# Kernel optimization log

Measured on AMD Instinct MI355X. Metric: run time of the kernel, lower is better.

Reference implementation:

```python
import jax, jax.numpy as jnp
import numpy as np

EMBED_DIM = 1024
NUM_HEADS = 16
HEAD_DIM = EMBED_DIM // NUM_HEADS
B, T = 2, 2048


def setup_inputs() -> dict:
    key = jax.random.key(0)
    ks = jax.random.split(key, 9)
    s = 1.0 / np.sqrt(EMBED_DIM)
    return {
        "x": jax.random.normal(ks[0], (B, T, EMBED_DIM), dtype=jnp.float32),
        "W_q": jax.random.uniform(ks[1], (EMBED_DIM, EMBED_DIM), jnp.float32, -s, s),
        "b_q": jax.random.uniform(ks[2], (EMBED_DIM,), jnp.float32, -s, s),
        "W_k": jax.random.uniform(ks[3], (EMBED_DIM, EMBED_DIM), jnp.float32, -s, s),
        "b_k": jax.random.uniform(ks[4], (EMBED_DIM,), jnp.float32, -s, s),
        "W_v": jax.random.uniform(ks[5], (EMBED_DIM, EMBED_DIM), jnp.float32, -s, s),
        "b_v": jax.random.uniform(ks[6], (EMBED_DIM,), jnp.float32, -s, s),
        "W_o": jax.random.uniform(ks[7], (EMBED_DIM, EMBED_DIM), jnp.float32, -s, s),
        "b_o": jax.random.uniform(ks[8], (EMBED_DIM,), jnp.float32, -s, s),
    }


def reference(x, W_q, b_q, W_k, b_k, W_v, b_v, W_o, b_o):
    Bv, Tv, C = x.shape
    # QKV projections (torch Linear: x @ W.T + b); split into heads -> (B,H,T,Dh)
    def proj(W, b):
        return (x @ W.T + b).reshape(Bv, Tv, NUM_HEADS, HEAD_DIM).transpose(0, 2, 1, 3)
    q, k, v = proj(W_q, b_q), proj(W_k, b_k), proj(W_v, b_v)
    scale = 1.0 / np.sqrt(HEAD_DIM).astype(np.float32)
    scores = jnp.einsum("bhqd,bhkd->bhqk", q, k) * scale  # (B,H,T,T)
    causal = jnp.tril(jnp.ones((Tv, Tv), dtype=bool))
    scores = jnp.where(causal, scores, -jnp.inf)
    attn = jax.nn.softmax(scores, axis=-1)
    # dropout is identity in eval / p=0
    out = jnp.einsum("bhqk,bhkd->bhqd", attn, v)  # (B,H,T,Dh)
    out = out.transpose(0, 2, 1, 3).reshape(Bv, Tv, C)
    return out @ W_o.T + b_o
```

## Files before the change

### kernel.cpp

```cpp
#include <hip/hip_runtime.h>
#include <hip/hip_bf16.h>


typedef __bf16 bf16;
typedef __attribute__((ext_vector_type(8))) __bf16 bf16x8;
typedef __attribute__((ext_vector_type(4))) __bf16 bf16x4;
typedef __attribute__((ext_vector_type(4))) float floatx4;
typedef __attribute__((ext_vector_type(8))) unsigned short us8;
typedef __attribute__((ext_vector_type(4))) unsigned short us4;

#define LOG2E 1.44269504088896340736f

__device__ __forceinline__ void gl2lds16(const void* g, void* l) {
  __builtin_amdgcn_global_load_lds((const __attribute__((address_space(1))) void*)g,
                                   (__attribute__((address_space(3))) void*)l, 16, 0, 0);
}

__global__ __launch_bounds__(256) void cast_all(
    const float* __restrict__ x, const float* __restrict__ wq,
    const float* __restrict__ wk, const float* __restrict__ wv,
    const float* __restrict__ wo, bf16* __restrict__ dst)
{
  const size_t M1 = (size_t)1 << 20;
  size_t i4 = ((size_t)blockIdx.x * 256 + threadIdx.x) * 4;
  const float* src = x;
  size_t off = i4;
  if (i4 >= 4 * M1) {
    size_t r = i4 - 4 * M1;
    int seg = (int)(r >> 20);
    off = r & (M1 - 1);
    src = (seg == 0) ? wq : (seg == 1) ? wk : (seg == 2) ? wv : wo;
  }
  float4 f = *(const float4*)(src + off);
  bf16x4 o = { (bf16)f.x, (bf16)f.y, (bf16)f.z, (bf16)f.w };
  *(bf16x4*)(dst + i4) = o;
}

template<bool F32OUT, bool QKV, int BN>
__global__ __launch_bounds__(256, 2) void gemm_bt(
    const bf16* __restrict__ A, const bf16* __restrict__ Wb,
    const float* __restrict__ bq, const float* __restrict__ bk,
    const float* __restrict__ bv, void* __restrict__ outb,
    int M, int N, int K, float qscale)
{
  __shared__ bf16 As[128 * 32];
  __shared__ bf16 Bs[BN * 32];
  const int tid = threadIdx.x;
  const int lane = tid & 63;
  const int wid = tid >> 6;
  const int l15 = lane & 15, l4 = lane >> 4;
  constexpr int I = (BN == 128) ? 4 : 2;
  const int wr = (BN == 128) ? (wid >> 1) : wid;
  const int wc = (BN == 128) ? (wid & 1) : 0;

  const bf16* W;
  const float* bias;
  float osc = 1.0f;
  int n0;
  bf16* outh;
  float* outf;
  if (QKV) {
    int mat = blockIdx.x >> 3;
    n0 = (blockIdx.x & 7) << 7;
    W = Wb + ((size_t)mat << 20);
    bias = (mat == 0) ? bq : (mat == 1 ? bk : bv);
    if (mat == 0) osc = qscale;
    outh = (bf16*)outb + ((size_t)mat << 22);
    outf = nullptr;
  } else {
    n0 = blockIdx.x * BN;
    W = Wb;
    bias = bq;
    outf = (float*)outb;
    outh = nullptr;
  }
  const int m0 = blockIdx.y << 7;

  floatx4 acc[I][4] = {};

  for (int k0 = 0; k0 < K; k0 += 32) {
#pragma unroll
    for (int it = 0; it < 2; ++it) {
      int c = it * 256 + tid;
      int row = c >> 2, kof = (c & 3) << 3;
      gl2lds16(A + (size_t)(m0 + row) * K + k0 + kof, As + c * 8);
    }
#pragma unroll
    for (int it = 0; it < BN / 64; ++it) {
      int c = it * 256 + tid;
      int row = c >> 2, kof = (c & 3) << 3;
      gl2lds16(W + (size_t)(n0 + row) * K + k0 + kof, Bs + c * 8);
    }
    __syncthreads();
    bf16x8 af[I], bfr[4];
#pragma unroll
    for (int i = 0; i < I; ++i)
      af[i] = *(const bf16x8*)(As + (wr * (I * 16) + i * 16 + l15) * 32 + l4 * 8);
#pragma unroll
    for (int j = 0; j < 4; ++j)
      bfr[j] = *(const bf16x8*)(Bs + (wc * 64 + j * 16 + l15) * 32 + l4 * 8);
#pragma unroll
    for (int i = 0; i < I; ++i)
#pragma unroll
      for (int j = 0; j < 4; ++j)
        acc[i][j] = __builtin_amdgcn_mfma_f32_16x16x32_bf16(af[i], bfr[j], acc[i][j], 0, 0, 0);
    __syncthreads();
  }

#pragma unroll
  for (int j = 0; j < 4; ++j) {
    int col = n0 + wc * 64 + j * 16 + l15;
    float bv_ = bias[col];
#pragma unroll
    for (int i = 0; i < I; ++i) {
#pragma unroll
      for (int rg = 0; rg < 4; ++rg) {
        int row = m0 + wr * (I * 16) + i * 16 + l4 * 4 + rg;
        float v = (acc[i][j][rg] + bv_) * osc;
        if (F32OUT) outf[(size_t)row * N + col] = v;
        else        outh[(size_t)row * N + col] = (bf16)v;
      }
    }
  }
}

__global__ __launch_bounds__(256) void transpose_v(
    const bf16* __restrict__ V, bf16* __restrict__ Vt)
{
  __shared__ bf16 tile[64 * 68];
  const int tid = threadIdx.x;
  const int t0 = blockIdx.x << 6;
  const int bh = blockIdx.y;
  const bf16* vp = V + ((size_t)(bh >> 4) * 2048) * 1024 + (bh & 15) * 64;
  bf16* op = Vt + ((size_t)bh << 17);

#pragma unroll
  for (int it = 0; it < 2; ++it) {
    int c = it * 256 + tid;
    int row = c >> 3, gcol = (c & 7) * 8;
    bf16x8 v8 = *(const bf16x8*)(vp + (size_t)(t0 + row) * 1024 + gcol);
    *(us4*)(&tile[row * 68 + gcol])     = *(us4*)&v8;
    *(us4*)(&tile[row * 68 + gcol + 4]) = ((us4*)&v8)[1];
  }
  __syncthreads();
#pragma unroll
  for (int it = 0; it < 2; ++it) {
    int u = it * 256 + tid;
    int d = u >> 3, ch = u & 7;
    us8 r;
#pragma unroll
    for (int jj = 0; jj < 8; ++jj)
      r[jj] = *(const unsigned short*)&tile[(ch * 8 + jj) * 68 + d];
    *(us8*)(op + (size_t)d * 2048 + t0 + ch * 8) = r;
  }
}

__global__ __launch_bounds__(256, 3) void attn_kernel(
    const bf16* __restrict__ Q, const bf16* __restrict__ Kg,
    const bf16* __restrict__ Vt, bf16* __restrict__ AO)
{
  constexpr int T = 2048, C = 1024;
  __shared__ bf16 Ks[2][64 * 64];
  __shared__ bf16 Vts[2][64 * 64];
  __shared__ bf16 Ps[4][16 * 72];

  const int tid = threadIdx.x;
  const int lane = tid & 63;
  const int w = tid >> 6;
  const int l15 = lane & 15, l4 = lane >> 4;

  const int p = blockIdx.x;
  const int bh = blockIdx.y;
  const size_t base = ((size_t)(bh >> 4) * T) * C + (bh & 15) * 64;
  const bf16* vtb = Vt + ((size_t)bh << 17);

  const bf16 one_h = (bf16)1.0f;
  const bf16x8 ones = {one_h, one_h, one_h, one_h, one_h, one_h, one_h, one_h};

  auto stageK = [&](int j0, int bufi) {
#pragma unroll
    for (int it = 0; it < 2; ++it) {
      int c = it * 256 + tid;
      int row = c >> 3, s = (c & 7) ^ (row & 7);
      gl2lds16(Kg + base + (size_t)(j0 + row) * C + s * 8, &Ks[bufi][c * 8]);
    }
  };
  auto stageV = [&](int j0, int bufi) {
#pragma unroll
    for (int it = 0; it < 2; ++it) {
      int c = it * 256 + tid;
      int row = c >> 3, s = (c & 7) ^ (row & 7);
      gl2lds16(vtb + ((size_t)row << 11) + j0 + s * 8, &Vts[bufi][c * 8]);
    }
  };

  const int qts[2] = { p, 31 - p };
  int g = 0;
  stageK(0, 0);
  stageV(0, 0);

  for (int seg = 0; seg < 2; ++seg) {
    const int qt = qts[seg];
    const int q0 = qt << 6;
    const int nkt = qt + 1;

    bf16x8 aq[2];
    {
      const bf16* qp = Q + base + (size_t)(q0 + w * 16 + l15) * C + l4 * 8;
      aq[0] = *(const bf16x8*)(qp);
      aq[1] = *(const bf16x8*)(qp + 32);
    }
    floatx4 o[4] = {};
    floatx4 lacc = {0.f, 0.f, 0.f, 0.f};
    float mrow[4] = {-1e38f, -1e38f, -1e38f, -1e38f};

    for (int jt = 0; jt < nkt; ++jt, ++g) {
      __syncthreads();
      const int cur = g & 1;
      if (jt + 1 < nkt) {
        stageK((jt + 1) << 6, cur ^ 1);
        stageV((jt + 1) << 6, cur ^ 1);
      } else if (seg == 0) {
        stageK(0, cur ^ 1);
        stageV(0, cur ^ 1);
      }

      floatx4 s4[4] = {};
#pragma unroll
      for (int kk = 0; kk < 2; ++kk) {
        bf16x8 bk8[4];
#pragma unroll
        for (int tj = 0; tj < 4; ++tj) {
          int r = tj * 16 + l15;
          int sl = (kk * 4 + l4) ^ (r & 7);
          bk8[tj] = *(const bf16x8*)(&Ks[cur][r * 64 + sl * 8]);
        }
#pragma unroll
        for (int tj = 0; tj < 4; ++tj)
          s4[tj] = __builtin_amdgcn_mfma_f32_16x16x32_bf16(aq[kk], bk8[tj], s4[tj], 0, 0, 0);
      }

      if (jt == nkt - 1) {
        const int j0 = jt << 6;
        int qrowb = q0 + w * 16 + l4 * 4;
#pragma unroll
        for (int tj = 0; tj < 4; ++tj) {
          int kcol = j0 + tj * 16 + l15;
#pragma unroll
          for (int rg = 0; rg < 4; ++rg)
            if (kcol > qrowb + rg) s4[tj][rg] = -3e38f;
        }
      }

#pragma unroll
      for (int rg = 0; rg < 4; ++rg) {
        float mx = fmaxf(fmaxf(s4[0][rg], s4[1][rg]), fmaxf(s4[2][rg], s4[3][rg]));
#pragma unroll
        for (int off = 1; off < 16; off <<= 1)
          mx = fmaxf(mx, __shfl_xor(mx, off, 64));
        float mnew = fmaxf(mrow[rg], mx);
        float al = __builtin_amdgcn_exp2f(mrow[rg] - mnew);
        mrow[rg] = mnew;
#pragma unroll
        for (int tj = 0; tj < 4; ++tj)
          s4[tj][rg] = __builtin_amdgcn_exp2f(s4[tj][rg] - mnew);
        lacc[rg] *= al;
#pragma unroll
        for (int td = 0; td < 4; ++td)
          o[td][rg] *= al;
      }

#pragma unroll
      for (int tj = 0; tj < 4; ++tj)
#pragma unroll
        for (int rg = 0; rg < 4; ++rg)
          Ps[w][(l4 * 4 + rg) * 72 + tj * 16 + l15] = (bf16)s4[tj][rg];

#pragma unroll
      for (int tk = 0; tk < 2; ++tk) {
        bf16x8 ap = *(const bf16x8*)(&Ps[w][l15 * 72 + tk * 32 + l4 * 8]);
        lacc = __builtin_amdgcn_mfma_f32_16x16x32_bf16(ap, ones, lacc, 0, 0, 0);
#pragma unroll
        for (int td = 0; td < 4; ++td) {
          int r = td * 16 + l15;
          int sl = (tk * 4 + l4) ^ (r & 7);
          bf16x8 bv8 = *(const bf16x8*)(&Vts[cur][r * 64 + sl * 8]);
          o[td] = __builtin_amdgcn_mfma_f32_16x16x32_bf16(ap, bv8, o[td], 0, 0, 0);
        }
      }
    }

#pragma unroll
    for (int rg = 0; rg < 4; ++rg) {
      float inv = 1.0f / lacc[rg];
      int qrow = q0 + w * 16 + l4 * 4 + rg;
#pragma unroll
      for (int td = 0; td < 4; ++td)
        AO[base + (size_t)qrow * C + td * 16 + l15] = (bf16)(o[td][rg] * inv);
    }
  }
}

extern "C" void kernel_launch(void* const* d_in, const int* in_sizes, int n_in,
                              void* d_out, int out_size, void* d_ws, size_t ws_size,
                              hipStream_t stream) {
  const float* x  = (const float*)d_in[0];
  const float* Wq = (const float*)d_in[1];
  const float* bq = (const float*)d_in[2];
  const float* Wk = (const float*)d_in[3];
  const float* bk = (const float*)d_in[4];
  const float* Wv = (const float*)d_in[5];
  const float* bv = (const float*)d_in[6];
  const float* Wo = (const float*)d_in[7];
  const float* bo = (const float*)d_in[8];

  bf16* ws = (bf16*)d_ws;
  const size_t M1 = (size_t)1 << 20;
  bf16* xb  = ws;
  bf16* Vtp = ws;
  bf16* wqb = ws + 4 * M1;
  bf16* wob = ws + 7 * M1;
  bf16* Qp  = ws + 8 * M1;
  bf16* AOp = ws + 20 * M1;

  cast_all<<<8192, 256, 0, stream>>>(x, Wq, Wk, Wv, Wo, ws);
  gemm_bt<false, true, 128><<<dim3(24, 32), 256, 0, stream>>>(
      xb, wqb, bq, bk, bv, (void*)Qp, 4096, 1024, 1024, 0.125f * LOG2E);
  transpose_v<<<dim3(32, 32), 256, 0, stream>>>(Qp + 8 * M1, Vtp);
  attn_kernel<<<dim3(16, 32), 256, 0, stream>>>(Qp, Qp + 4 * M1, Vtp, AOp);
  gemm_bt<true, false, 64><<<dim3(16, 32), 256, 0, stream>>>(
      AOp, wob, bo, nullptr, nullptr, d_out, 4096, 1024, 1024, 1.0f);
}
```

Before: 206.9 us.

## Use 128-row query tiles per block with transposed S MFMA and register row sums

The attention kernel now gives each block one 128-row query tile, so each wave handles 32 query rows, instead of pairing two 64-row tiles per block. Each staged K/V tile is reused by twice as many query rows. Blocks are ordered longest-first to balance the causal workload. S is computed as K·Q^T so each lane holds a query column, which lets row max and sum use two shuffles and accumulate the sum in registers instead of using a ones-MFMA. The cost is more registers (launch bounds lowered from 3 to 2 blocks per CU) and waves that sit idle on fully masked tiles.

```diff
diff --git a/kernel.cpp b/kernel.cpp
--- a/kernel.cpp
+++ b/kernel.cpp
@@ -155,27 +155,39 @@
   }
 }
 
-__global__ __launch_bounds__(256, 3) void attn_kernel(
+__global__ __launch_bounds__(256, 2) void attn_kernel(
     const bf16* __restrict__ Q, const bf16* __restrict__ Kg,
     const bf16* __restrict__ Vt, bf16* __restrict__ AO)
 {
   constexpr int T = 2048, C = 1024;
   __shared__ bf16 Ks[2][64 * 64];
   __shared__ bf16 Vts[2][64 * 64];
-  __shared__ bf16 Ps[4][16 * 72];
+  __shared__ bf16 Ps[4][32 * 72];
 
   const int tid = threadIdx.x;
   const int lane = tid & 63;
   const int w = tid >> 6;
   const int l15 = lane & 15, l4 = lane >> 4;
 
-  const int p = blockIdx.x;
-  const int bh = blockIdx.y;
+  const int u = blockIdx.x;
+  const int bh = u & 31;
+  const int p = u >> 5;
+  const int qt = (p < 8) ? (15 - p) : (p - 8);
+  const int q0 = qt << 7;
   const size_t base = ((size_t)(bh >> 4) * T) * C + (bh & 15) * 64;
   const bf16* vtb = Vt + ((size_t)bh << 17);
 
-  const bf16 one_h = (bf16)1.0f;
-  const bf16x8 ones = {one_h, one_h, one_h, one_h, one_h, one_h, one_h, one_h};
+  bf16x8 qf[2][2];
+#pragma unroll
+  for (int tq = 0; tq < 2; ++tq) {
+    const bf16* qp = Q + base + (size_t)(q0 + w * 32 + tq * 16 + l15) * C + l4 * 8;
+    qf[tq][0] = *(const bf16x8*)(qp);
+    qf[tq][1] = *(const bf16x8*)(qp + 32);
+  }
+
+  floatx4 o[2][4] = {};
+  float mrow[2] = {-1e38f, -1e38f};
+  float lrow[2] = {0.f, 0.f};
 
   auto stageK = [&](int j0, int bufi) {
 #pragma unroll
@@ -194,111 +206,128 @@
     }
   };
 
-  const int qts[2] = { p, 31 - p };
-  int g = 0;
+  const int nkt = 2 * qt + 2;
   stageK(0, 0);
   stageV(0, 0);
 
-  for (int seg = 0; seg < 2; ++seg) {
-    const int qt = qts[seg];
-    const int q0 = qt << 6;
-    const int nkt = qt + 1;
-
-    bf16x8 aq[2];
-    {
-      const bf16* qp = Q + base + (size_t)(q0 + w * 16 + l15) * C + l4 * 8;
-      aq[0] = *(const bf16x8*)(qp);
-      aq[1] = *(const bf16x8*)(qp + 32);
-    }
-    floatx4 o[4] = {};
-    floatx4 lacc = {0.f, 0.f, 0.f, 0.f};
-    float mrow[4] = {-1e38f, -1e38f, -1e38f, -1e38f};
-
-    for (int jt = 0; jt < nkt; ++jt, ++g) {
-      __syncthreads();
-      const int cur = g & 1;
-      if (jt + 1 < nkt) {
-        stageK((jt + 1) << 6, cur ^ 1);
-        stageV((jt + 1) << 6, cur ^ 1);
-      } else if (seg == 0) {
-        stageK(0, cur ^ 1);
-        stageV(0, cur ^ 1);
-      }
-
-      floatx4 s4[4] = {};
+  for (int jt = 0; jt < nkt; ++jt) {
+    __syncthreads();
+    const int cur = jt & 1;
+    if (jt + 1 < nkt) {
+      stageK((jt + 1) << 6, cur ^ 1);
+      stageV((jt + 1) << 6, cur ^ 1);
+    }
+    const int j0 = jt << 6;
+    const int qwave = q0 + w * 32;
+    if (j0 <= qwave + 31) {
+      floatx4 s4[4][2] = {};
 #pragma unroll
       for (int kk = 0; kk < 2; ++kk) {
-        bf16x8 bk8[4];
+        bf16x8 kf[4];
 #pragma unroll
         for (int tj = 0; tj < 4; ++tj) {
           int r = tj * 16 + l15;
           int sl = (kk * 4 + l4) ^ (r & 7);
-          bk8[tj] = *(const bf16x8*)(&Ks[cur][r * 64 + sl * 8]);
+          kf[tj] = *(const bf16x8*)(&Ks[cur][r * 64 + sl * 8]);
         }
 #pragma unroll
         for (int tj = 0; tj < 4; ++tj)
-          s4[tj] = __builtin_amdgcn_mfma_f32_16x16x32_bf16(aq[kk], bk8[tj], s4[tj], 0, 0, 0);
-      }
-
-      if (jt == nkt - 1) {
-        const int j0 = jt << 6;
-        int qrowb = q0 + w * 16 + l4 * 4;
+#pragma unroll
+          for (int tq = 0; tq < 2; ++tq)
+            s4[tj][tq] = __builtin_amdgcn_mfma_f32_16x16x32_bf16(kf[tj], qf[tq][kk], s4[tj][tq], 0, 0, 0);
+      }
+
+      if (j0 + 63 > qwave) {
 #pragma unroll
         for (int tj = 0; tj < 4; ++tj) {
-          int kcol = j0 + tj * 16 + l15;
+          int j = j0 + tj * 16 + l4 * 4;
+#pragma unroll
+          for (int tq = 0; tq < 2; ++tq) {
+            int q = qwave + tq * 16 + l15;
+#pragma unroll
+            for (int rg = 0; rg < 4; ++rg)
+              if (j + rg > q) s4[tj][tq][rg] = -3e38f;
+          }
+        }
+      }
+
+      float al[2];
+#pragma unroll
+      for (int tq = 0; tq < 2; ++tq) {
+        float mx = -3e38f;
+#pragma unroll
+        for (int tj = 0; tj < 4; ++tj)
 #pragma unroll
           for (int rg = 0; rg < 4; ++rg)
-            if (kcol > qrowb + rg) s4[tj][rg] = -3e38f;
-        }
-      }
-
-#pragma unroll
-      for (int rg = 0; rg < 4; ++rg) {
-        float mx = fmaxf(fmaxf(s4[0][rg], s4[1][rg]), fmaxf(s4[2][rg], s4[3][rg]));
-#pragma unroll
-        for (int off = 1; off < 16; off <<= 1)
-          mx = fmaxf(mx, __shfl_xor(mx, off, 64));
-        float mnew = fmaxf(mrow[rg], mx);
-        float al = __builtin_amdgcn_exp2f(mrow[rg] - mnew);
-        mrow[rg] = mnew;
+            mx = fmaxf(mx, s4[tj][tq][rg]);
+        mx = fmaxf(mx, __shfl_xor(mx, 16, 64));
+        mx = fmaxf(mx, __shfl_xor(mx, 32, 64));
+        float mnew = fmaxf(mrow[tq], mx);
+        al[tq] = __builtin_amdgcn_exp2f(mrow[tq] - mnew);
+        mrow[tq] = mnew;
+        float psum = 0.f;
 #pragma unroll
         for (int tj = 0; tj < 4; ++tj)
-          s4[tj][rg] = __builtin_amdgcn_exp2f(s4[tj][rg] - mnew);
-        lacc[rg] *= al;
-#pragma unroll
-        for (int td = 0; td < 4; ++td)
-          o[td][rg] *= al;
-      }
-
-#pragma unroll
-      for (int tj = 0; tj < 4; ++tj)
-#pragma unroll
-        for (int rg = 0; rg < 4; ++rg)
-          Ps[w][(l4 * 4 + rg) * 72 + tj * 16 + l15] = (bf16)s4[tj][rg];
+#pragma unroll
+          for (int rg = 0; rg < 4; ++rg) {
+            float e = __builtin_amdgcn_exp2f(s4[tj][tq][rg] - mnew);
+            s4[tj][tq][rg] = e;
+            psum += e;
+          }
+        psum += __shfl_xor(psum, 16, 64);
+        psum += __shfl_xor(psum, 32, 64);
+        lrow[tq] = lrow[tq] * al[tq] + psum;
+      }
+
+#pragma unroll
+      for (int tq = 0; tq < 2; ++tq)
+#pragma unroll
+        for (int tj = 0; tj < 4; ++tj) {
+          bf16x4 pk = { (bf16)s4[tj][tq][0], (bf16)s4[tj][tq][1],
+                        (bf16)s4[tj][tq][2], (bf16)s4[tj][tq][3] };
+          *(bf16x4*)(&Ps[w][(tq * 16 + l15) * 72 + tj * 16 + l4 * 4]) = pk;
+        }
+
+#pragma unroll
+      for (int tm = 0; tm < 2; ++tm)
+#pragma unroll
+        for (int rg = 0; rg < 4; ++rg) {
+          float aO = __shfl(al[tm], l4 * 4 + rg, 64);
+#pragma unroll
+          for (int td = 0; td < 4; ++td)
+            o[tm][td][rg] *= aO;
+        }
 
 #pragma unroll
       for (int tk = 0; tk < 2; ++tk) {
-        bf16x8 ap = *(const bf16x8*)(&Ps[w][l15 * 72 + tk * 32 + l4 * 8]);
-        lacc = __builtin_amdgcn_mfma_f32_16x16x32_bf16(ap, ones, lacc, 0, 0, 0);
+        bf16x8 pf[2];
+#pragma unroll
+        for (int tm = 0; tm < 2; ++tm)
+          pf[tm] = *(const bf16x8*)(&Ps[w][(tm * 16 + l15) * 72 + tk * 32 + l4 * 8]);
 #pragma unroll
         for (int td = 0; td < 4; ++td) {
           int r = td * 16 + l15;
           int sl = (tk * 4 + l4) ^ (r & 7);
-          bf16x8 bv8 = *(const bf16x8*)(&Vts[cur][r * 64 + sl * 8]);
-          o[td] = __builtin_amdgcn_mfma_f32_16x16x32_bf16(ap, bv8, o[td], 0, 0, 0);
-        }
-      }
-    }
-
+          bf16x8 vf = *(const bf16x8*)(&Vts[cur][r * 64 + sl * 8]);
+#pragma unroll
+          for (int tm = 0; tm < 2; ++tm)
+            o[tm][td] = __builtin_amdgcn_mfma_f32_16x16x32_bf16(pf[tm], vf, o[tm][td], 0, 0, 0);
+        }
+      }
+    }
+  }
+
+  float inv[2] = { 1.0f / lrow[0], 1.0f / lrow[1] };
+#pragma unroll
+  for (int tm = 0; tm < 2; ++tm)
 #pragma unroll
     for (int rg = 0; rg < 4; ++rg) {
-      float inv = 1.0f / lacc[rg];
-      int qrow = q0 + w * 16 + l4 * 4 + rg;
+      float iv = __shfl(inv[tm], l4 * 4 + rg, 64);
+      int qrow = q0 + w * 32 + tm * 16 + l4 * 4 + rg;
 #pragma unroll
       for (int td = 0; td < 4; ++td)
-        AO[base + (size_t)qrow * C + td * 16 + l15] = (bf16)(o[td][rg] * inv);
-    }
-  }
+        AO[base + (size_t)qrow * C + td * 16 + l15] = (bf16)(o[tm][td][rg] * iv);
+    }
 }
 
 extern "C" void kernel_launch(void* const* d_in, const int* in_sizes, int n_in,
@@ -327,7 +356,7 @@
   gemm_bt<false, true, 128><<<dim3(24, 32), 256, 0, stream>>>(
       xb, wqb, bq, bk, bv, (void*)Qp, 4096, 1024, 1024, 0.125f * LOG2E);
   transpose_v<<<dim3(32, 32), 256, 0, stream>>>(Qp + 8 * M1, Vtp);
-  attn_kernel<<<dim3(16, 32), 256, 0, stream>>>(Qp, Qp + 4 * M1, Vtp, AOp);
+  attn_kernel<<<512, 256, 0, stream>>>(Qp, Qp + 4 * M1, Vtp, AOp);
   gemm_bt<true, false, 64><<<dim3(16, 32), 256, 0, stream>>>(
       AOp, wob, bo, nullptr, nullptr, d_out, 4096, 1024, 1024, 1.0f);
 }
```

Result: no change. 204.4 us (-1.2%).

## Fuse V transpose into QKV GEMM epilogue and restructure attention grid

Applied to the files above, without the earlier changes.

The QKV projection GEMM now writes the V output directly in transposed per-head layout, which removes the separate transpose kernel launch and its extra read and write of V. The attention kernel swaps its paired-q-tile work assignment for one q-tile per block over 1024 blocks, longest tiles first. It also computes S^T and O^T with swapped MFMA operands so row statistics reduce with two shuffles, and it replaces the ones-MFMA row sum with register sums. The risks are strided 8-byte scattered stores for Vt in the GEMM epilogue and load imbalance without tile pairing.

```diff
diff --git a/kernel.cpp b/kernel.cpp
--- a/kernel.cpp
+++ b/kernel.cpp
@@ -6,8 +6,6 @@
 typedef __attribute__((ext_vector_type(8))) __bf16 bf16x8;
 typedef __attribute__((ext_vector_type(4))) __bf16 bf16x4;
 typedef __attribute__((ext_vector_type(4))) float floatx4;
-typedef __attribute__((ext_vector_type(8))) unsigned short us8;
-typedef __attribute__((ext_vector_type(4))) unsigned short us4;
 
 #define LOG2E 1.44269504088896340736f
 
@@ -41,7 +39,7 @@
     const bf16* __restrict__ A, const bf16* __restrict__ Wb,
     const float* __restrict__ bq, const float* __restrict__ bk,
     const float* __restrict__ bv, void* __restrict__ outb,
-    int M, int N, int K, float qscale)
+    bf16* __restrict__ vt, int M, int N, int K, float qscale)
 {
   __shared__ bf16 As[128 * 32];
   __shared__ bf16 Bs[BN * 32];
@@ -56,11 +54,11 @@
   const bf16* W;
   const float* bias;
   float osc = 1.0f;
-  int n0;
+  int n0, mat = 0;
   bf16* outh;
   float* outf;
   if (QKV) {
-    int mat = blockIdx.x >> 3;
+    mat = blockIdx.x >> 3;
     n0 = (blockIdx.x & 7) << 7;
     W = Wb + ((size_t)mat << 20);
     bias = (mat == 0) ? bq : (mat == 1 ? bk : bv);
@@ -107,6 +105,25 @@
     __syncthreads();
   }
 
+  if (QKV && mat == 2) {
+#pragma unroll
+    for (int j = 0; j < 4; ++j) {
+      int col = n0 + wc * 64 + j * 16 + l15;
+      float bv_ = bias[col];
+      int h = col >> 6, d = col & 63;
+#pragma unroll
+      for (int i = 0; i < I; ++i) {
+        int row = m0 + wr * (I * 16) + i * 16 + l4 * 4;
+        int bb = row >> 11, t = row & 2047;
+        bf16x4 pk;
+#pragma unroll
+        for (int rg = 0; rg < 4; ++rg) pk[rg] = (bf16)(acc[i][j][rg] + bv_);
+        *(bf16x4*)(vt + (((size_t)(bb * 16 + h)) << 17) + ((size_t)d << 11) + t) = pk;
+      }
+    }
+    return;
+  }
+
 #pragma unroll
   for (int j = 0; j < 4; ++j) {
     int col = n0 + wc * 64 + j * 16 + l15;
@@ -121,37 +138,6 @@
         else        outh[(size_t)row * N + col] = (bf16)v;
       }
     }
-  }
-}
-
-__global__ __launch_bounds__(256) void transpose_v(
-    const bf16* __restrict__ V, bf16* __restrict__ Vt)
-{
-  __shared__ bf16 tile[64 * 68];
-  const int tid = threadIdx.x;
-  const int t0 = blockIdx.x << 6;
-  const int bh = blockIdx.y;
-  const bf16* vp = V + ((size_t)(bh >> 4) * 2048) * 1024 + (bh & 15) * 64;
-  bf16* op = Vt + ((size_t)bh << 17);
-
-#pragma unroll
-  for (int it = 0; it < 2; ++it) {
-    int c = it * 256 + tid;
-    int row = c >> 3, gcol = (c & 7) * 8;
-    bf16x8 v8 = *(const bf16x8*)(vp + (size_t)(t0 + row) * 1024 + gcol);
-    *(us4*)(&tile[row * 68 + gcol])     = *(us4*)&v8;
-    *(us4*)(&tile[row * 68 + gcol + 4]) = ((us4*)&v8)[1];
-  }
-  __syncthreads();
-#pragma unroll
-  for (int it = 0; it < 2; ++it) {
-    int u = it * 256 + tid;
-    int d = u >> 3, ch = u & 7;
-    us8 r;
-#pragma unroll
-    for (int jj = 0; jj < 8; ++jj)
-      r[jj] = *(const unsigned short*)&tile[(ch * 8 + jj) * 68 + d];
-    *(us8*)(op + (size_t)d * 2048 + t0 + ch * 8) = r;
   }
 }
 
@@ -162,20 +148,31 @@
   constexpr int T = 2048, C = 1024;
   __shared__ bf16 Ks[2][64 * 64];
   __shared__ bf16 Vts[2][64 * 64];
-  __shared__ bf16 Ps[4][16 * 72];
+  __shared__ bf16 Ps[4][16 * 80];
 
   const int tid = threadIdx.x;
   const int lane = tid & 63;
   const int w = tid >> 6;
   const int l15 = lane & 15, l4 = lane >> 4;
 
-  const int p = blockIdx.x;
-  const int bh = blockIdx.y;
+  const int u = blockIdx.x;
+  const int bh = u & 31;
+  const int qt = 31 - (u >> 5);
+  const int q0 = qt << 6;
   const size_t base = ((size_t)(bh >> 4) * T) * C + (bh & 15) * 64;
   const bf16* vtb = Vt + ((size_t)bh << 17);
 
-  const bf16 one_h = (bf16)1.0f;
-  const bf16x8 ones = {one_h, one_h, one_h, one_h, one_h, one_h, one_h, one_h};
+  const int q = q0 + w * 16 + l15;
+
+  bf16x8 qf[2];
+  {
+    const bf16* qp = Q + base + (size_t)q * C + l4 * 8;
+    qf[0] = *(const bf16x8*)(qp);
+    qf[1] = *(const bf16x8*)(qp + 32);
+  }
+
+  floatx4 o[4] = {};
+  float mrow = -1e38f, lrow = 0.f;
 
   auto stageK = [&](int j0, int bufi) {
 #pragma unroll
@@ -194,110 +191,100 @@
     }
   };
 
-  const int qts[2] = { p, 31 - p };
-  int g = 0;
+  const int nkt = qt + 1;
   stageK(0, 0);
   stageV(0, 0);
 
-  for (int seg = 0; seg < 2; ++seg) {
-    const int qt = qts[seg];
-    const int q0 = qt << 6;
-    const int nkt = qt + 1;
-
-    bf16x8 aq[2];
-    {
-      const bf16* qp = Q + base + (size_t)(q0 + w * 16 + l15) * C + l4 * 8;
-      aq[0] = *(const bf16x8*)(qp);
-      aq[1] = *(const bf16x8*)(qp + 32);
-    }
-    floatx4 o[4] = {};
-    floatx4 lacc = {0.f, 0.f, 0.f, 0.f};
-    float mrow[4] = {-1e38f, -1e38f, -1e38f, -1e38f};
-
-    for (int jt = 0; jt < nkt; ++jt, ++g) {
-      __syncthreads();
-      const int cur = g & 1;
-      if (jt + 1 < nkt) {
-        stageK((jt + 1) << 6, cur ^ 1);
-        stageV((jt + 1) << 6, cur ^ 1);
-      } else if (seg == 0) {
-        stageK(0, cur ^ 1);
-        stageV(0, cur ^ 1);
-      }
-
-      floatx4 s4[4] = {};
-#pragma unroll
-      for (int kk = 0; kk < 2; ++kk) {
-        bf16x8 bk8[4];
-#pragma unroll
-        for (int tj = 0; tj < 4; ++tj) {
-          int r = tj * 16 + l15;
-          int sl = (kk * 4 + l4) ^ (r & 7);
-          bk8[tj] = *(const bf16x8*)(&Ks[cur][r * 64 + sl * 8]);
-        }
-#pragma unroll
-        for (int tj = 0; tj < 4; ++tj)
-          s4[tj] = __builtin_amdgcn_mfma_f32_16x16x32_bf16(aq[kk], bk8[tj], s4[tj], 0, 0, 0);
-      }
-
-      if (jt == nkt - 1) {
-        const int j0 = jt << 6;
-        int qrowb = q0 + w * 16 + l4 * 4;
-#pragma unroll
-        for (int tj = 0; tj < 4; ++tj) {
-          int kcol = j0 + tj * 16 + l15;
-#pragma unroll
-          for (int rg = 0; rg < 4; ++rg)
-            if (kcol > qrowb + rg) s4[tj][rg] = -3e38f;
-        }
-      }
-
+  for (int jt = 0; jt < nkt; ++jt) {
+    __syncthreads();
+    const int cur = jt & 1;
+    if (jt + 1 < nkt) {
+      stageK((jt + 1) << 6, cur ^ 1);
+      stageV((jt + 1) << 6, cur ^ 1);
+    }
+    const int j0 = jt << 6;
+
+    floatx4 s4[4] = {};
+#pragma unroll
+    for (int kk = 0; kk < 2; ++kk) {
+      bf16x8 kf[4];
+#pragma unroll
+      for (int tj = 0; tj < 4; ++tj) {
+        int r = tj * 16 + l15;
+        int sl = (kk * 4 + l4) ^ (r & 7);
+        kf[tj] = *(const bf16x8*)(&Ks[cur][r * 64 + sl * 8]);
+      }
+#pragma unroll
+      for (int tj = 0; tj < 4; ++tj)
+        s4[tj] = __builtin_amdgcn_mfma_f32_16x16x32_bf16(kf[tj], qf[kk], s4[tj], 0, 0, 0);
+    }
+
+    if (jt == nkt - 1) {
+#pragma unroll
+      for (int tj = 0; tj < 4; ++tj) {
+        int j = j0 + tj * 16 + l4 * 4;
+#pragma unroll
+        for (int rg = 0; rg < 4; ++rg)
+          if (j + rg > q) s4[tj][rg] = -3e38f;
+      }
+    }
+
+    float mx = -3e38f;
+#pragma unroll
+    for (int tj = 0; tj < 4; ++tj)
+#pragma unroll
+      for (int rg = 0; rg < 4; ++rg)
+        mx = fmaxf(mx, s4[tj][rg]);
+    mx = fmaxf(mx, __shfl_xor(mx, 16, 64));
+    mx = fmaxf(mx, __shfl_xor(mx, 32, 64));
+    float mnew = fmaxf(mrow, mx);
+    float al = __builtin_amdgcn_exp2f(mrow - mnew);
+    mrow = mnew;
+    float psum = 0.f;
+#pragma unroll
+    for (int tj = 0; tj < 4; ++tj)
 #pragma unroll
       for (int rg = 0; rg < 4; ++rg) {
-        float mx = fmaxf(fmaxf(s4[0][rg], s4[1][rg]), fmaxf(s4[2][rg], s4[3][rg]));
-#pragma unroll
-        for (int off = 1; off < 16; off <<= 1)
-          mx = fmaxf(mx, __shfl_xor(mx, off, 64));
-        float mnew = fmaxf(mrow[rg], mx);
-        float al = __builtin_amdgcn_exp2f(mrow[rg] - mnew);
-        mrow[rg] = mnew;
-#pragma unroll
-        for (int tj = 0; tj < 4; ++tj)
-          s4[tj][rg] = __builtin_amdgcn_exp2f(s4[tj][rg] - mnew);
-        lacc[rg] *= al;
-#pragma unroll
-        for (int td = 0; td < 4; ++td)
-          o[td][rg] *= al;
-      }
-
-#pragma unroll
-      for (int tj = 0; tj < 4; ++tj)
-#pragma unroll
-        for (int rg = 0; rg < 4; ++rg)
-          Ps[w][(l4 * 4 + rg) * 72 + tj * 16 + l15] = (bf16)s4[tj][rg];
-
-#pragma unroll
-      for (int tk = 0; tk < 2; ++tk) {
-        bf16x8 ap = *(const bf16x8*)(&Ps[w][l15 * 72 + tk * 32 + l4 * 8]);
-        lacc = __builtin_amdgcn_mfma_f32_16x16x32_bf16(ap, ones, lacc, 0, 0, 0);
-#pragma unroll
-        for (int td = 0; td < 4; ++td) {
-          int r = td * 16 + l15;
-          int sl = (tk * 4 + l4) ^ (r & 7);
-          bf16x8 bv8 = *(const bf16x8*)(&Vts[cur][r * 64 + sl * 8]);
-          o[td] = __builtin_amdgcn_mfma_f32_16x16x32_bf16(ap, bv8, o[td], 0, 0, 0);
-        }
-      }
-    }
-
-#pragma unroll
-    for (int rg = 0; rg < 4; ++rg) {
-      float inv = 1.0f / lacc[rg];
-      int qrow = q0 + w * 16 + l4 * 4 + rg;
-#pragma unroll
-      for (int td = 0; td < 4; ++td)
-        AO[base + (size_t)qrow * C + td * 16 + l15] = (bf16)(o[td][rg] * inv);
-    }
+        float e = __builtin_amdgcn_exp2f(s4[tj][rg] - mnew);
+        s4[tj][rg] = e;
+        psum += e;
+      }
+    psum += __shfl_xor(psum, 16, 64);
+    psum += __shfl_xor(psum, 32, 64);
+    lrow = lrow * al + psum;
+
+#pragma unroll
+    for (int tj = 0; tj < 4; ++tj) {
+      bf16x4 pk = { (bf16)s4[tj][0], (bf16)s4[tj][1],
+                    (bf16)s4[tj][2], (bf16)s4[tj][3] };
+      *(bf16x4*)(&Ps[w][l15 * 80 + tj * 16 + l4 * 4]) = pk;
+    }
+
+#pragma unroll
+    for (int td = 0; td < 4; ++td)
+#pragma unroll
+      for (int rg = 0; rg < 4; ++rg)
+        o[td][rg] *= al;
+
+#pragma unroll
+    for (int tk = 0; tk < 2; ++tk) {
+      bf16x8 pf = *(const bf16x8*)(&Ps[w][l15 * 80 + tk * 32 + l4 * 8]);
+#pragma unroll
+      for (int td = 0; td < 4; ++td) {
+        int r = td * 16 + l15;
+        int sl = (tk * 4 + l4) ^ (r & 7);
+        bf16x8 vf = *(const bf16x8*)(&Vts[cur][r * 64 + sl * 8]);
+        o[td] = __builtin_amdgcn_mfma_f32_16x16x32_bf16(vf, pf, o[td], 0, 0, 0);
+      }
+    }
+  }
+
+  float inv = 1.0f / lrow;
+#pragma unroll
+  for (int td = 0; td < 4; ++td) {
+    bf16x4 ok = { (bf16)(o[td][0] * inv), (bf16)(o[td][1] * inv),
+                  (bf16)(o[td][2] * inv), (bf16)(o[td][3] * inv) };
+    *(bf16x4*)(AO + base + (size_t)q * C + td * 16 + l4 * 4) = ok;
   }
 }
 
@@ -317,17 +304,16 @@
   bf16* ws = (bf16*)d_ws;
   const size_t M1 = (size_t)1 << 20;
   bf16* xb  = ws;
-  bf16* Vtp = ws;
   bf16* wqb = ws + 4 * M1;
   bf16* wob = ws + 7 * M1;
   bf16* Qp  = ws + 8 * M1;
+  bf16* Vtp = ws + 16 * M1;
   bf16* AOp = ws + 20 * M1;
 
   cast_all<<<8192, 256, 0, stream>>>(x, Wq, Wk, Wv, Wo, ws);
   gemm_bt<false, true, 128><<<dim3(24, 32), 256, 0, stream>>>(
-      xb, wqb, bq, bk, bv, (void*)Qp, 4096, 1024, 1024, 0.125f * LOG2E);
-  transpose_v<<<dim3(32, 32), 256, 0, stream>>>(Qp + 8 * M1, Vtp);
-  attn_kernel<<<dim3(16, 32), 256, 0, stream>>>(Qp, Qp + 4 * M1, Vtp, AOp);
+      xb, wqb, bq, bk, bv, (void*)Qp, Vtp, 4096, 1024, 1024, 0.125f * LOG2E);
+  attn_kernel<<<1024, 256, 0, stream>>>(Qp, Qp + 4 * M1, Vtp, AOp);
   gemm_bt<true, false, 64><<<dim3(16, 32), 256, 0, stream>>>(
-      AOp, wob, bo, nullptr, nullptr, d_out, 4096, 1024, 1024, 1.0f);
-}
+      AOp, wob, bo, nullptr, nullptr, d_out, nullptr, 4096, 1024, 1024, 1.0f);
+}
```

After: 185.8 us. 10.2% less time.
